# Performance work log

Hardware: AMD Instinct MI355X
Metric: run time of the kernel (lower is better)

The kernel has to match this reference:

```python
import jax, jax.numpy as jnp
import numpy as np

H = 256       # hiddenDim
E = 300       # embDim
VOCAB = 50000
S = 1024      # number of sentences in document
L = 64        # words per sentence (chain-tree depth)
TOPIC = 100
TARGET = 5


def setup_inputs() -> dict:
    key = jax.random.key(0)
    ks = jax.random.split(key, 21)
    f32 = jnp.float32
    return {
        'sentenceInIndex': jax.random.randint(ks[0], (S, L), 0, VOCAB),
        'depTypes': jax.random.randint(ks[1], (S, L - 1), 0, 9),
        'D_T_distr': jax.random.uniform(ks[2], (TOPIC,), dtype=f32),
        'h0': jax.random.normal(ks[3], (H,), dtype=f32),
        'idx2vec': jax.random.normal(ks[4], (VOCAB, E), dtype=f32) * 0.1,
        'q': jax.random.normal(ks[5], (10, H), dtype=f32) * 0.1,
        'W': jax.random.normal(ks[6], (3 * H, E), dtype=f32) * 0.05,
        'U': jax.random.normal(ks[7], (3 * H, H), dtype=f32) * 0.05,
        'D': jax.random.normal(ks[8], (3 * H, H), dtype=f32) * 0.05,
        'b': jax.random.normal(ks[9], (3 * H,), dtype=f32) * 0.05,
        'gru_wih': jax.random.normal(ks[10], (3 * H, H), dtype=f32) * 0.05,
        'gru_whh': jax.random.normal(ks[11], (3 * H, H), dtype=f32) * 0.05,
        'gru_bih': jax.random.normal(ks[12], (3 * H,), dtype=f32) * 0.05,
        'gru_bhh': jax.random.normal(ks[13], (3 * H,), dtype=f32) * 0.05,
        'gate_W': jax.random.normal(ks[14], (2 * H, H), dtype=f32) * 0.05,
        'gate_U': jax.random.normal(ks[15], (2 * H, H), dtype=f32) * 0.05,
        'gate_b': jax.random.normal(ks[16], (2 * H,), dtype=f32) * 0.05,
        'mlp_W': jax.random.normal(ks[17], (H, TOPIC), dtype=f32) * 0.05,
        'mlp_b': jax.random.normal(ks[18], (H,), dtype=f32) * 0.05,
        'out_W': jax.random.normal(ks[19], (TARGET, H), dtype=f32) * 0.05,
        'out_b': jax.random.normal(ks[20], (TARGET,), dtype=f32) * 0.05,
    }


def reference(sentenceInIndex, depTypes, D_T_distr, h0, idx2vec, q, W, U, D, b,
              gru_wih, gru_whh, gru_bih, gru_bhh,
              gate_W, gate_U, gate_b, mlp_W, mlp_b, out_W, out_b):
    # ---- DERNN over chain-canonicalized dependency trees (vectorized over S sentences) ----
    x = idx2vec[sentenceInIndex]                        # [S, L, E] gather
    Wx = jnp.einsum('sle,ke->slk', x, W)                # [S, L, 3H]
    qe = q[depTypes]                                    # [S, L-1, H] dep-type embeddings for edges k->k+1
    Dq = jnp.einsum('slh,kh->slk', qe, D)               # [S, L-1, 3H]

    # leaf node (position L-1): q_sum = q[-1] ('leafNotion'); no child h term
    dq_leaf = D @ q[-1]                                 # [3H]
    iu_leaf = Wx[:, -1, H:] + dq_leaf[H:] + b[H:]       # [S, 2H]
    h = jnp.tanh(jax.nn.sigmoid(iu_leaf[:, :H]) * jnp.tanh(iu_leaf[:, H:]))  # [S, H]

    # internal nodes k = L-2 .. 0, single child k+1 (edge k)
    pre = Wx[:, :L - 1] + Dq + b                        # [S, L-1, 3H]
    pre_rev = jnp.swapaxes(pre[:, ::-1], 0, 1)          # [L-1, S, 3H] bottom-up order

    def tree_step(h_c, pre_k):
        tot = pre_k + h_c @ U.T                         # [S, 3H]
        f = jax.nn.sigmoid(tot[:, :H]) * h_c            # child forget gate * child h (single child => sum)
        i = jax.nn.sigmoid(tot[:, H:2 * H])
        u = jnp.tanh(tot[:, 2 * H:])
        h_n = jnp.tanh(i * u + f)
        return h_n, None

    sentenceVector, _ = jax.lax.scan(tree_step, h, pre_rev)  # [S, H] root hidden per sentence

    # ---- GRU over sentence sequence (batch 1), torch nn.GRU math ----
    def gru_step(hh, xt):
        gi = gru_wih @ xt + gru_bih                     # [3H]
        gh = gru_whh @ hh + gru_bhh
        r = jax.nn.sigmoid(gi[:H] + gh[:H])
        z = jax.nn.sigmoid(gi[H:2 * H] + gh[H:2 * H])
        n = jnp.tanh(gi[2 * H:] + r * gh[2 * H:])
        return (1.0 - z) * n + z * hh, None

    hT, _ = jax.lax.scan(gru_step, h0, sentenceVector)  # [H] final hidden state

    # ---- topic vector, GATE fusion, classifier ----
    t = jnp.tanh(mlp_W @ D_T_distr + mlp_b)             # [H]
    g = gate_W @ hT + gate_U @ t + gate_b               # [2H]
    v = jnp.tanh(jax.nn.sigmoid(g[:H]) * hT + jax.nn.sigmoid(g[H:]) * t)
    return jax.nn.softmax(out_W @ v + out_b)            # [TARGET]
```

## Files before the change

kernel.cpp:

```cpp
#include <hip/hip_runtime.h>

typedef short short8 __attribute__((ext_vector_type(8)));
typedef float f4 __attribute__((ext_vector_type(4)));
typedef int i4 __attribute__((ext_vector_type(4)));
typedef _Float16 half8 __attribute__((ext_vector_type(8)));
typedef _Float16 h2 __attribute__((ext_vector_type(2)));

#define HD 256
#define ED 300
#define EP 320
#define TH 768
#define NS 1024
#define LW 64
#define SH 4.5f

__device__ __forceinline__ unsigned short f2bf(float f) {
    unsigned int u = __float_as_uint(f);
    u = (u + 0x7FFFu + ((u >> 16) & 1u)) >> 16;
    return (unsigned short)u;
}
__device__ __forceinline__ float bf2f(unsigned short s) {
    return __uint_as_float(((unsigned int)s) << 16);
}
__device__ __forceinline__ float sigm(float x) {
    return __builtin_amdgcn_rcpf(1.f + __expf(-x));
}
__device__ __forceinline__ float tanh_(float x) {
    x = fminf(fmaxf(x, -15.f), 15.f);
    return 1.f - 2.f * __builtin_amdgcn_rcpf(1.f + __expf(2.f * x));
}
__device__ __forceinline__ unsigned int pack_h2(float a, float b) {
    h2 p; p.x = (_Float16)a; p.y = (_Float16)b;
    return __builtin_bit_cast(unsigned int, p);
}

__device__ __forceinline__ void load8bf(const unsigned short* p, float* o) {
    uint4 a = *(const uint4*)p;
    o[0] = bf2f((unsigned short)(a.x & 0xffff)); o[1] = bf2f((unsigned short)(a.x >> 16));
    o[2] = bf2f((unsigned short)(a.y & 0xffff)); o[3] = bf2f((unsigned short)(a.y >> 16));
    o[4] = bf2f((unsigned short)(a.z & 0xffff)); o[5] = bf2f((unsigned short)(a.z >> 16));
    o[6] = bf2f((unsigned short)(a.w & 0xffff)); o[7] = bf2f((unsigned short)(a.w >> 16));
}
__device__ __forceinline__ void ubf4(uint2 a, float* o) {
    o[0] = bf2f((unsigned short)(a.x & 0xffff)); o[1] = bf2f((unsigned short)(a.x >> 16));
    o[2] = bf2f((unsigned short)(a.y & 0xffff)); o[3] = bf2f((unsigned short)(a.y >> 16));
}

__global__ void k_prep(const float* __restrict__ W, const float* __restrict__ U,
                       const float* __restrict__ Wih, const float* __restrict__ Whh,
                       const float* __restrict__ q, const float* __restrict__ Dm,
                       const float* __restrict__ DT, const float* __restrict__ mlpW,
                       const float* __restrict__ mlpb,
                       const float* __restrict__ bih, const float* __restrict__ bhh,
                       unsigned short* __restrict__ Wb, _Float16* __restrict__ Uh,
                       _Float16* __restrict__ Wihh,
                       signed char* __restrict__ Wq, float* __restrict__ rowscale,
                       float* __restrict__ bias2,
                       float* __restrict__ Dq, float* __restrict__ tv) {
    __shared__ float smax[4];
    int bid = blockIdx.x, tid = threadIdx.x;
    if (bid < 768) {
        int r = bid;
        for (int j = tid; j < EP; j += 256)
            Wb[r * EP + j] = (j < ED) ? f2bf(W[r * ED + j]) : (unsigned short)0;
        float whv = Whh[r * HD + tid];
        for (int j = tid; j < HD; j += 256) {
            Uh[r * HD + j] = (_Float16)U[r * HD + j];
            Wihh[r * HD + j] = (_Float16)Wih[r * HD + j];
        }
        float v = fabsf(whv);
        for (int o = 32; o; o >>= 1) v = fmaxf(v, __shfl_xor(v, o));
        if ((tid & 63) == 0) smax[tid >> 6] = v;
        __syncthreads();
        float am = fmaxf(fmaxf(smax[0], smax[1]), fmaxf(smax[2], smax[3]));
        float inv = (am > 0.f) ? 127.f / am : 0.f;
        int qi = (int)rintf(whv * inv);
        qi = max(-127, min(127, qi));
        Wq[r * HD + tid] = (signed char)qi;
        if (tid == 0) rowscale[r] = (am / 127.f) * (SH / 127.f);
    } else if (bid < 798) {
        int idx = bid - 768;
        int d = idx / 3, part = idx - d * 3;
        int n = part * 256 + tid;
        float s = 0.f;
        for (int h = 0; h < HD; ++h) s += Dm[n * HD + h] * q[d * HD + h];
        Dq[d * TH + n] = s;
    } else {
        if (tid < HD) {
            float s = 0.f;
            for (int k = 0; k < 100; ++k) s += mlpW[tid * 100 + k] * DT[k];
            tv[tid] = tanh_(s + mlpb[tid]);
        }
        for (int r = tid; r < TH; r += 256)
            bias2[r] = bih[r] + ((r < 512) ? bhh[r] : 0.f);
    }
}

#define XP 328
__launch_bounds__(256, 2)
__global__ void k_phaseB(const int* __restrict__ sIdx, const int* __restrict__ depT,
                         const float* __restrict__ emb, const unsigned short* __restrict__ Wb,
                         const float* __restrict__ Dq, const float* __restrict__ bias,
                         unsigned short* __restrict__ pre) {
    __shared__ float dq_s[10 * 772];
    __shared__ float b_s[TH];
    __shared__ int dep_s[32];
    __shared__ int idx_s[32];
    __shared__ __align__(16) unsigned short xbf[32 * XP];
    int tid = threadIdx.x;
    int c0 = blockIdx.x * 32;
    for (int i = tid; i < 10 * 768; i += 256) {
        int d = i / 768, n = i - d * 768;
        dq_s[d * 772 + n] = Dq[i];
    }
    for (int i = tid; i < TH; i += 256) b_s[i] = bias[i];
    if (tid < 32) {
        int m = c0 + tid;
        idx_s[tid] = sIdx[m];
        int l = m & 63, s = m >> 6;
        dep_s[tid] = (l == 63) ? 9 : depT[s * 63 + l];
    }
    __syncthreads();
    for (int i = tid; i < 32 * EP; i += 256) {
        int row = i / EP, col = i - row * EP;
        unsigned short v = 0;
        if (col < ED) v = f2bf(emb[(long)idx_s[row] * ED + col]);
        xbf[row * XP + col] = v;
    }
    __syncthreads();

    int lane = tid & 63;
    int w = tid >> 6;
    int quad = lane >> 4, l16 = lane & 15;

    f4 acc[2][12];
#pragma unroll
    for (int cs = 0; cs < 2; ++cs)
#pragma unroll
        for (int ms = 0; ms < 12; ++ms) acc[cs][ms] = (f4){0.f, 0.f, 0.f, 0.f};

    const unsigned short* wbase = Wb + (w * 192 + l16) * EP;

#pragma unroll
    for (int kt = 0; kt < 10; ++kt) {
        int k0 = kt * 32 + quad * 8;
        short8 bf0 = *(const short8*)&xbf[l16 * XP + k0];
        short8 bf1 = *(const short8*)&xbf[(16 + l16) * XP + k0];
#pragma unroll
        for (int ms = 0; ms < 12; ++ms) {
            short8 af = *(const short8*)(wbase + ms * 16 * EP + k0);
            acc[0][ms] = __builtin_amdgcn_mfma_f32_16x16x32_bf16(af, bf0, acc[0][ms], 0, 0, 0);
            acc[1][ms] = __builtin_amdgcn_mfma_f32_16x16x32_bf16(af, bf1, acc[1][ms], 0, 0, 0);
        }
    }

#pragma unroll
    for (int cs = 0; cs < 2; ++cs) {
        int xr = c0 + cs * 16 + l16;
        int dep = dep_s[cs * 16 + l16];
        unsigned short* prow = pre + (long)xr * TH;
#pragma unroll
        for (int ms = 0; ms < 12; ++ms) {
            int ncol = w * 192 + ms * 16 + quad * 4;
            f4 dq4 = *(const f4*)&dq_s[dep * 772 + ncol];
            f4 b4 = *(const f4*)&b_s[ncol];
            unsigned int lo = (unsigned int)f2bf(acc[cs][ms][0] + dq4[0] + b4[0]) |
                              ((unsigned int)f2bf(acc[cs][ms][1] + dq4[1] + b4[1]) << 16);
            unsigned int hi = (unsigned int)f2bf(acc[cs][ms][2] + dq4[2] + b4[2]) |
                              ((unsigned int)f2bf(acc[cs][ms][3] + dq4[3] + b4[3]) << 16);
            uint2 v; v.x = lo; v.y = hi;
            *(uint2*)(prow + ncol) = v;
        }
    }
}

__global__ void __launch_bounds__(768) k_phaseC(
                         const unsigned short* __restrict__ pre,
                         const _Float16* __restrict__ Uh,
                         const _Float16* __restrict__ Wihh,
                         const float* __restrict__ bias2,
                         float* __restrict__ gi) {
    __shared__ __align__(16) uint4 hfr[512];
    __shared__ __align__(16) float tot[16 * 772];
    int tid = threadIdx.x;
    int lane = tid & 63, w = tid >> 6, quad = lane >> 4, l16 = lane & 15;
    int s0 = blockIdx.x * 16;

    uint4 frag[32];
    {
        const _Float16* base = Uh + (w * 64 + l16) * HD;
#pragma unroll
        for (int t = 0; t < 4; ++t)
#pragma unroll
            for (int kt = 0; kt < 8; ++kt)
                frag[t * 8 + kt] = *(const uint4*)(base + t * 16 * HD + kt * 32 + quad * 8);
    }

    int us = tid >> 5;
    int jg = tid & 31;
    int j0 = jg * 8;
    int hcell = (j0 >> 5) * 64 + 16 * ((j0 >> 3) & 3) + us;
    uint4 hcp;

    if (tid < 512) {
        const unsigned short* prow = pre + ((long)(s0 + us) * LW + 63) * TH;
        float iv[8], uv[8], hcv[8];
        load8bf(prow + 256 + j0, iv);
        load8bf(prow + 512 + j0, uv);
#pragma unroll
        for (int r = 0; r < 8; ++r) hcv[r] = tanh_(sigm(iv[r]) * tanh_(uv[r]));
        hcp.x = pack_h2(hcv[0], hcv[1]); hcp.y = pack_h2(hcv[2], hcv[3]);
        hcp.z = pack_h2(hcv[4], hcv[5]); hcp.w = pack_h2(hcv[6], hcv[7]);
        hfr[hcell] = hcp;
    }
    __syncthreads();

    int mb = w * 64 + quad * 4;

    for (int step = 0; step < 63; ++step) {
        int l = 62 - step;
        uint2 praw[6];
        if (tid < 512) {
            const unsigned short* prow = pre + ((long)(s0 + us) * LW + l) * TH;
#pragma unroll
            for (int g = 0; g < 3; ++g) {
                praw[2 * g]     = *(const uint2*)(prow + g * 256 + j0);
                praw[2 * g + 1] = *(const uint2*)(prow + g * 256 + j0 + 4);
            }
        }
        f4 a0 = (f4){0,0,0,0}, a1 = (f4){0,0,0,0}, a2 = (f4){0,0,0,0}, a3 = (f4){0,0,0,0};
#pragma unroll
        for (int kt = 0; kt < 8; ++kt) {
            half8 b = __builtin_bit_cast(half8, hfr[kt * 64 + lane]);
            a0 = __builtin_amdgcn_mfma_f32_16x16x32_f16(__builtin_bit_cast(half8, frag[kt]), b, a0, 0, 0, 0);
            a1 = __builtin_amdgcn_mfma_f32_16x16x32_f16(__builtin_bit_cast(half8, frag[8 + kt]), b, a1, 0, 0, 0);
            a2 = __builtin_amdgcn_mfma_f32_16x16x32_f16(__builtin_bit_cast(half8, frag[16 + kt]), b, a2, 0, 0, 0);
            a3 = __builtin_amdgcn_mfma_f32_16x16x32_f16(__builtin_bit_cast(half8, frag[24 + kt]), b, a3, 0, 0, 0);
        }
        float* tr = tot + l16 * 772;
        *(f4*)&tr[mb] = a0;
        *(f4*)&tr[mb + 16] = a1;
        *(f4*)&tr[mb + 32] = a2;
        *(f4*)&tr[mb + 48] = a3;
        __syncthreads();
        if (tid < 512) {
            const float* ts = tot + us * 772;
            float hcv[8];
            h2 px = __builtin_bit_cast(h2, hcp.x); h2 py = __builtin_bit_cast(h2, hcp.y);
            h2 pz = __builtin_bit_cast(h2, hcp.z); h2 pw = __builtin_bit_cast(h2, hcp.w);
            hcv[0] = (float)px.x; hcv[1] = (float)px.y; hcv[2] = (float)py.x; hcv[3] = (float)py.y;
            hcv[4] = (float)pz.x; hcv[5] = (float)pz.y; hcv[6] = (float)pw.x; hcv[7] = (float)pw.y;
#pragma unroll
            for (int hf = 0; hf < 2; ++hf) {
                int jb = j0 + hf * 4;
                float pf[4], pi_[4], pu[4];
                ubf4(praw[hf], pf);
                ubf4(praw[2 + hf], pi_);
                ubf4(praw[4 + hf], pu);
                f4 tf = *(const f4*)&ts[jb];
                f4 ti = *(const f4*)&ts[256 + jb];
                f4 tu = *(const f4*)&ts[512 + jb];
#pragma unroll
                for (int r = 0; r < 4; ++r) {
                    float ff = tf[r] + pf[r];
                    float ii = ti[r] + pi_[r];
                    float uu = tu[r] + pu[r];
                    hcv[hf * 4 + r] = tanh_(sigm(ii) * tanh_(uu) + sigm(ff) * hcv[hf * 4 + r]);
                }
            }
            hcp.x = pack_h2(hcv[0], hcv[1]); hcp.y = pack_h2(hcv[2], hcv[3]);
            hcp.z = pack_h2(hcv[4], hcv[5]); hcp.w = pack_h2(hcv[6], hcv[7]);
            hfr[hcell] = hcp;
        }
        __syncthreads();
    }

    {
        const _Float16* base = Wihh + (w * 64 + l16) * HD;
#pragma unroll
        for (int t = 0; t < 4; ++t)
#pragma unroll
            for (int kt = 0; kt < 8; ++kt)
                frag[t * 8 + kt] = *(const uint4*)(base + t * 16 * HD + kt * 32 + quad * 8);
    }
    f4 a0 = (f4){0,0,0,0}, a1 = (f4){0,0,0,0}, a2 = (f4){0,0,0,0}, a3 = (f4){0,0,0,0};
#pragma unroll
    for (int kt = 0; kt < 8; ++kt) {
        half8 b = __builtin_bit_cast(half8, hfr[kt * 64 + lane]);
        a0 = __builtin_amdgcn_mfma_f32_16x16x32_f16(__builtin_bit_cast(half8, frag[kt]), b, a0, 0, 0, 0);
        a1 = __builtin_amdgcn_mfma_f32_16x16x32_f16(__builtin_bit_cast(half8, frag[8 + kt]), b, a1, 0, 0, 0);
        a2 = __builtin_amdgcn_mfma_f32_16x16x32_f16(__builtin_bit_cast(half8, frag[16 + kt]), b, a2, 0, 0, 0);
        a3 = __builtin_amdgcn_mfma_f32_16x16x32_f16(__builtin_bit_cast(half8, frag[24 + kt]), b, a3, 0, 0, 0);
    }
    float* go = gi + (long)(s0 + l16) * TH;
    f4 b0 = *(const f4*)(bias2 + mb);
    f4 b1 = *(const f4*)(bias2 + mb + 16);
    f4 b2 = *(const f4*)(bias2 + mb + 32);
    f4 b3 = *(const f4*)(bias2 + mb + 48);
    *(f4*)(go + mb) = a0 + b0;
    *(f4*)(go + mb + 16) = a1 + b1;
    *(f4*)(go + mb + 32) = a2 + b2;
    *(f4*)(go + mb + 48) = a3 + b3;
}

__global__ void __launch_bounds__(512) k_gru(
                      const signed char* __restrict__ Wq, const float* __restrict__ rowscale,
                      const float* __restrict__ bhh,
                      const float* __restrict__ gi, const float* __restrict__ h0,
                      const float* __restrict__ tv,
                      const float* __restrict__ gateW, const float* __restrict__ gateU,
                      const float* __restrict__ gateb,
                      const float* __restrict__ outW, const float* __restrict__ outb,
                      float* __restrict__ out) {
    __shared__ __align__(16) signed char qbuf[2][HD];
    __shared__ float hts[HD];
    __shared__ float sgs[512];
    __shared__ float vvs[HD];
    __shared__ float lg[8];

    int tid = threadIdx.x;
    int lane = tid & 63, w = tid >> 6, quad = lane >> 4, l16 = lane & 15;

    i4 far_[2][4], faz[2][4], fan[2][4];
#pragma unroll
    for (int c = 0; c < 2; ++c) {
        const signed char* qr_ = Wq + (long)(w * 32 + c * 16 + l16) * HD;
        const signed char* qz_ = Wq + (long)(256 + w * 32 + c * 16 + l16) * HD;
        const signed char* qn_ = Wq + (long)(512 + w * 32 + c * 16 + l16) * HD;
#pragma unroll
        for (int kc = 0; kc < 4; ++kc) {
            far_[c][kc] = *(const i4*)(qr_ + kc * 64 + quad * 16);
            faz[c][kc] = *(const i4*)(qz_ + kc * 64 + quad * 16);
            fan[c][kc] = *(const i4*)(qn_ + kc * 64 + quad * 16);
        }
    }

    int sc = (l16 >> 2) & 1;
    int sr = l16 & 3;
    int j = w * 32 + sc * 16 + quad * 4 + sr;
    bool b2 = (sr & 2) != 0, b1 = (sr & 1) != 0, bc = (sc != 0);
    bool owner = (l16 < 8);

    float rs_r = rowscale[j];
    float rs_z = rowscale[256 + j];
    float rs_n = rowscale[512 + j];
    float bn_l = bhh[512 + j];

    float hv = h0[j];
    if (owner) {
        float hc = fminf(fmaxf(hv, -SH), SH);
        qbuf[0][j] = (signed char)(int)rintf(hc * (127.f / SH));
    }
    __syncthreads();

    const float* gbase = gi + j;
    for (int t = 0; t < NS; ++t) {
        int p = t & 1;
        const float* g = gbase + (long)t * TH;
        float gr_l = g[0], gz_l = g[256], gn_l = g[512];

        i4 qr[2], qz[2], qn[2];
#pragma unroll
        for (int c = 0; c < 2; ++c) { qr[c] = (i4){0,0,0,0}; qz[c] = (i4){0,0,0,0}; qn[c] = (i4){0,0,0,0}; }
#pragma unroll
        for (int kc = 0; kc < 4; ++kc) {
            i4 b = *(const i4*)&qbuf[p][kc * 64 + quad * 16];
            qr[0] = __builtin_amdgcn_mfma_i32_16x16x64_i8(far_[0][kc], b, qr[0], 0, 0, 0);
            qr[1] = __builtin_amdgcn_mfma_i32_16x16x64_i8(far_[1][kc], b, qr[1], 0, 0, 0);
            qz[0] = __builtin_amdgcn_mfma_i32_16x16x64_i8(faz[0][kc], b, qz[0], 0, 0, 0);
            qz[1] = __builtin_amdgcn_mfma_i32_16x16x64_i8(faz[1][kc], b, qz[1], 0, 0, 0);
            qn[0] = __builtin_amdgcn_mfma_i32_16x16x64_i8(fan[0][kc], b, qn[0], 0, 0, 0);
            qn[1] = __builtin_amdgcn_mfma_i32_16x16x64_i8(fan[1][kc], b, qn[1], 0, 0, 0);
        }
        int ra0 = bc ? qr[1][0] : qr[0][0], ra1 = bc ? qr[1][1] : qr[0][1];
        int ra2 = bc ? qr[1][2] : qr[0][2], ra3 = bc ? qr[1][3] : qr[0][3];
        int rt0 = b2 ? ra2 : ra0, rt1 = b2 ? ra3 : ra1;
        int qrv = b1 ? rt1 : rt0;
        int za0 = bc ? qz[1][0] : qz[0][0], za1 = bc ? qz[1][1] : qz[0][1];
        int za2 = bc ? qz[1][2] : qz[0][2], za3 = bc ? qz[1][3] : qz[0][3];
        int zt0 = b2 ? za2 : za0, zt1 = b2 ? za3 : za1;
        int qzv = b1 ? zt1 : zt0;
        int na0 = bc ? qn[1][0] : qn[0][0], na1 = bc ? qn[1][1] : qn[0][1];
        int na2 = bc ? qn[1][2] : qn[0][2], na3 = bc ? qn[1][3] : qn[0][3];
        int nt0 = b2 ? na2 : na0, nt1 = b2 ? na3 : na1;
        int qnv = b1 ? nt1 : nt0;
        float rv = sigm(gr_l + (float)qrv * rs_r);
        float zv = sigm(gz_l + (float)qzv * rs_z);
        float nv = tanh_(gn_l + rv * ((float)qnv * rs_n + bn_l));
        hv = (1.f - zv) * nv + zv * hv;
        if (owner) {
            float hc = fminf(fmaxf(hv, -SH), SH);
            qbuf[p ^ 1][j] = (signed char)(int)rintf(hc * (127.f / SH));
        }
        __syncthreads();
    }

    if (owner) hts[j] = hv;
    __syncthreads();
    {
        float s = gateb[tid];
        for (int k = 0; k < HD; ++k)
            s += gateW[tid * HD + k] * hts[k] + gateU[tid * HD + k] * tv[k];
        sgs[tid] = sigm(s);
    }
    __syncthreads();
    if (tid < HD) vvs[tid] = tanh_(sgs[tid] * hts[tid] + sgs[256 + tid] * tv[tid]);
    __syncthreads();
    if (tid < 5) {
        float s = outb[tid];
        for (int k = 0; k < HD; ++k) s += outW[tid * HD + k] * vvs[k];
        lg[tid] = s;
    }
    __syncthreads();
    if (tid == 0) {
        float m = lg[0];
        for (int i = 1; i < 5; ++i) m = fmaxf(m, lg[i]);
        float e[5], sum = 0.f;
        for (int i = 0; i < 5; ++i) { e[i] = __expf(lg[i] - m); sum += e[i]; }
        for (int i = 0; i < 5; ++i) out[i] = e[i] / sum;
    }
}

extern "C" void kernel_launch(void* const* d_in, const int* in_sizes, int n_in,
                              void* d_out, int out_size, void* d_ws, size_t ws_size,
                              hipStream_t stream) {
    (void)in_sizes; (void)n_in; (void)out_size; (void)ws_size;
    const int* sIdx = (const int*)d_in[0];
    const int* depT = (const int*)d_in[1];
    const float* DT = (const float*)d_in[2];
    const float* h0 = (const float*)d_in[3];
    const float* emb = (const float*)d_in[4];
    const float* q = (const float*)d_in[5];
    const float* W = (const float*)d_in[6];
    const float* U = (const float*)d_in[7];
    const float* Dm = (const float*)d_in[8];
    const float* b = (const float*)d_in[9];
    const float* Wih = (const float*)d_in[10];
    const float* Whh = (const float*)d_in[11];
    const float* bih = (const float*)d_in[12];
    const float* bhh = (const float*)d_in[13];
    const float* gateW = (const float*)d_in[14];
    const float* gateU = (const float*)d_in[15];
    const float* gateb = (const float*)d_in[16];
    const float* mlpW = (const float*)d_in[17];
    const float* mlpb = (const float*)d_in[18];
    const float* outW = (const float*)d_in[19];
    const float* outb = (const float*)d_in[20];

    char* ws = (char*)d_ws;
    unsigned short* Wb = (unsigned short*)ws;   ws += 768 * 320 * 2;
    _Float16* Uh = (_Float16*)ws;               ws += 768 * 256 * 2;
    _Float16* Wihh = (_Float16*)ws;             ws += 768 * 256 * 2;
    signed char* Wq = (signed char*)ws;         ws += 768 * 256;
    float* rowscale = (float*)ws;               ws += 768 * 4;
    float* bias2 = (float*)ws;                  ws += 768 * 4;
    float* Dq = (float*)ws;                     ws += 10 * 768 * 4;
    float* tv = (float*)ws;                     ws += 1024;
    ws = (char*)d_ws + ((((size_t)(ws - (char*)d_ws)) + 4095) & ~(size_t)4095);
    unsigned short* pre = (unsigned short*)ws;  ws += (size_t)65536 * 768 * 2;
    float* gi = (float*)ws;                     ws += (size_t)1024 * 768 * 4;

    k_prep<<<dim3(799), dim3(256), 0, stream>>>(W, U, Wih, Whh, q, Dm, DT, mlpW, mlpb,
                                                bih, bhh,
                                                Wb, Uh, Wihh, Wq, rowscale, bias2, Dq, tv);
    k_phaseB<<<dim3(2048), dim3(256), 0, stream>>>(sIdx, depT, emb, Wb, Dq, b, pre);
    k_phaseC<<<dim3(64), dim3(768), 0, stream>>>(pre, Uh, Wihh, bias2, gi);
    k_gru<<<dim3(1), dim3(512), 0, stream>>>(Wq, rowscale, bhh, gi, h0, tv,
                                             gateW, gateU, gateb, outW, outb, (float*)d_out);
}
```

Baseline: 1.311 ms.

## Replace MFMA int8 GRU recurrence with per-row sdot4 dot products across 768 threads

```diff
diff --git a/kernel.cpp b/kernel.cpp
--- a/kernel.cpp
+++ b/kernel.cpp
@@ -44,6 +44,19 @@
 __device__ __forceinline__ void ubf4(uint2 a, float* o) {
     o[0] = bf2f((unsigned short)(a.x & 0xffff)); o[1] = bf2f((unsigned short)(a.x >> 16));
     o[2] = bf2f((unsigned short)(a.y & 0xffff)); o[3] = bf2f((unsigned short)(a.y >> 16));
+}
+
+__device__ __forceinline__ int dot4(int a, int b, int c) {
+#if __has_builtin(__builtin_amdgcn_sdot4)
+    return __builtin_amdgcn_sdot4(a, b, c, false);
+#else
+    int s = c;
+    s += (int)(signed char)(a & 0xff)        * (int)(signed char)(b & 0xff);
+    s += (int)(signed char)((a >> 8) & 0xff) * (int)(signed char)((b >> 8) & 0xff);
+    s += (int)(signed char)((a >> 16) & 0xff)* (int)(signed char)((b >> 16) & 0xff);
+    s += (int)(signed char)((a >> 24) & 0xff)* (int)(signed char)((b >> 24) & 0xff);
+    return s;
+#endif
 }
 
 __global__ void k_prep(const float* __restrict__ W, const float* __restrict__ U,
@@ -303,7 +316,7 @@
     *(f4*)(go + mb + 48) = a3 + b3;
 }
 
-__global__ void __launch_bounds__(512) k_gru(
+__global__ void __launch_bounds__(768) k_gru(
                       const signed char* __restrict__ Wq, const float* __restrict__ rowscale,
                       const float* __restrict__ bhh,
                       const float* __restrict__ gi, const float* __restrict__ h0,
@@ -312,92 +325,66 @@
                       const float* __restrict__ gateb,
                       const float* __restrict__ outW, const float* __restrict__ outb,
                       float* __restrict__ out) {
-    __shared__ __align__(16) signed char qbuf[2][HD];
+    __shared__ __align__(16) int qd[2][64];
+    __shared__ float sums[TH];
+    __shared__ float gns[HD];
     __shared__ float hts[HD];
     __shared__ float sgs[512];
     __shared__ float vvs[HD];
     __shared__ float lg[8];
 
     int tid = threadIdx.x;
-    int lane = tid & 63, w = tid >> 6, quad = lane >> 4, l16 = lane & 15;
-
-    i4 far_[2][4], faz[2][4], fan[2][4];
-#pragma unroll
-    for (int c = 0; c < 2; ++c) {
-        const signed char* qr_ = Wq + (long)(w * 32 + c * 16 + l16) * HD;
-        const signed char* qz_ = Wq + (long)(256 + w * 32 + c * 16 + l16) * HD;
-        const signed char* qn_ = Wq + (long)(512 + w * 32 + c * 16 + l16) * HD;
-#pragma unroll
-        for (int kc = 0; kc < 4; ++kc) {
-            far_[c][kc] = *(const i4*)(qr_ + kc * 64 + quad * 16);
-            faz[c][kc] = *(const i4*)(qz_ + kc * 64 + quad * 16);
-            fan[c][kc] = *(const i4*)(qn_ + kc * 64 + quad * 16);
-        }
-    }
-
-    int sc = (l16 >> 2) & 1;
-    int sr = l16 & 3;
-    int j = w * 32 + sc * 16 + quad * 4 + sr;
-    bool b2 = (sr & 2) != 0, b1 = (sr & 1) != 0, bc = (sc != 0);
-    bool owner = (l16 < 8);
-
-    float rs_r = rowscale[j];
-    float rs_z = rowscale[256 + j];
-    float rs_n = rowscale[512 + j];
-    float bn_l = bhh[512 + j];
-
-    float hv = h0[j];
+    int row = tid;
+    bool isn = (row >= 512);
+    bool owner = (row < HD);
+
+    i4 wv[16];
+    {
+        const signed char* wr = Wq + (long)row * HD;
+#pragma unroll
+        for (int c = 0; c < 16; ++c) wv[c] = *(const i4*)(wr + c * 16);
+    }
+    float rs = rowscale[row];
+    float bn = isn ? bhh[row] : 0.f;
+
+    float hv = owner ? h0[row] : 0.f;
     if (owner) {
         float hc = fminf(fmaxf(hv, -SH), SH);
-        qbuf[0][j] = (signed char)(int)rintf(hc * (127.f / SH));
-    }
-    __syncthreads();
-
-    const float* gbase = gi + j;
+        ((signed char*)qd[0])[row] = (signed char)(int)rintf(hc * (127.f / SH));
+    }
+    __syncthreads();
+
+    const float* gbase = gi + row;
     for (int t = 0; t < NS; ++t) {
         int p = t & 1;
-        const float* g = gbase + (long)t * TH;
-        float gr_l = g[0], gz_l = g[256], gn_l = g[512];
-
-        i4 qr[2], qz[2], qn[2];
-#pragma unroll
-        for (int c = 0; c < 2; ++c) { qr[c] = (i4){0,0,0,0}; qz[c] = (i4){0,0,0,0}; qn[c] = (i4){0,0,0,0}; }
-#pragma unroll
-        for (int kc = 0; kc < 4; ++kc) {
-            i4 b = *(const i4*)&qbuf[p][kc * 64 + quad * 16];
-            qr[0] = __builtin_amdgcn_mfma_i32_16x16x64_i8(far_[0][kc], b, qr[0], 0, 0, 0);
-            qr[1] = __builtin_amdgcn_mfma_i32_16x16x64_i8(far_[1][kc], b, qr[1], 0, 0, 0);
-            qz[0] = __builtin_amdgcn_mfma_i32_16x16x64_i8(faz[0][kc], b, qz[0], 0, 0, 0);
-            qz[1] = __builtin_amdgcn_mfma_i32_16x16x64_i8(faz[1][kc], b, qz[1], 0, 0, 0);
-            qn[0] = __builtin_amdgcn_mfma_i32_16x16x64_i8(fan[0][kc], b, qn[0], 0, 0, 0);
-            qn[1] = __builtin_amdgcn_mfma_i32_16x16x64_i8(fan[1][kc], b, qn[1], 0, 0, 0);
-        }
-        int ra0 = bc ? qr[1][0] : qr[0][0], ra1 = bc ? qr[1][1] : qr[0][1];
-        int ra2 = bc ? qr[1][2] : qr[0][2], ra3 = bc ? qr[1][3] : qr[0][3];
-        int rt0 = b2 ? ra2 : ra0, rt1 = b2 ? ra3 : ra1;
-        int qrv = b1 ? rt1 : rt0;
-        int za0 = bc ? qz[1][0] : qz[0][0], za1 = bc ? qz[1][1] : qz[0][1];
-        int za2 = bc ? qz[1][2] : qz[0][2], za3 = bc ? qz[1][3] : qz[0][3];
-        int zt0 = b2 ? za2 : za0, zt1 = b2 ? za3 : za1;
-        int qzv = b1 ? zt1 : zt0;
-        int na0 = bc ? qn[1][0] : qn[0][0], na1 = bc ? qn[1][1] : qn[0][1];
-        int na2 = bc ? qn[1][2] : qn[0][2], na3 = bc ? qn[1][3] : qn[0][3];
-        int nt0 = b2 ? na2 : na0, nt1 = b2 ? na3 : na1;
-        int qnv = b1 ? nt1 : nt0;
-        float rv = sigm(gr_l + (float)qrv * rs_r);
-        float zv = sigm(gz_l + (float)qzv * rs_z);
-        float nv = tanh_(gn_l + rv * ((float)qnv * rs_n + bn_l));
-        hv = (1.f - zv) * nv + zv * hv;
+        float gv = gbase[(long)t * TH];
+        int acc = 0;
+#pragma unroll
+        for (int c = 0; c < 16; ++c) {
+            i4 hb = *(const i4*)&qd[p][c * 4];
+            acc = dot4(hb[0], wv[c][0], acc);
+            acc = dot4(hb[1], wv[c][1], acc);
+            acc = dot4(hb[2], wv[c][2], acc);
+            acc = dot4(hb[3], wv[c][3], acc);
+        }
+        float fv = (float)acc * rs;
+        sums[row] = isn ? (fv + bn) : (fv + gv);
+        if (isn) gns[row - 512] = gv;
+        __syncthreads();
         if (owner) {
+            float rv = sigm(sums[row]);
+            float zv = sigm(sums[HD + row]);
+            float nv = tanh_(gns[row] + rv * sums[512 + row]);
+            hv = (1.f - zv) * nv + zv * hv;
             float hc = fminf(fmaxf(hv, -SH), SH);
-            qbuf[p ^ 1][j] = (signed char)(int)rintf(hc * (127.f / SH));
+            ((signed char*)qd[p ^ 1])[row] = (signed char)(int)rintf(hc * (127.f / SH));
         }
         __syncthreads();
     }
 
-    if (owner) hts[j] = hv;
-    __syncthreads();
-    {
+    if (owner) hts[row] = hv;
+    __syncthreads();
+    if (tid < 512) {
         float s = gateb[tid];
         for (int k = 0; k < HD; ++k)
             s += gateW[tid * HD + k] * hts[k] + gateU[tid * HD + k] * tv[k];
@@ -465,6 +452,6 @@
                                                 Wb, Uh, Wihh, Wq, rowscale, bias2, Dq, tv);
     k_phaseB<<<dim3(2048), dim3(256), 0, stream>>>(sIdx, depT, emb, Wb, Dq, b, pre);
     k_phaseC<<<dim3(64), dim3(768), 0, stream>>>(pre, Uh, Wihh, bias2, gi);
-    k_gru<<<dim3(1), dim3(512), 0, stream>>>(Wq, rowscale, bhh, gi, h0, tv,
+    k_gru<<<dim3(1), dim3(768), 0, stream>>>(Wq, rowscale, bhh, gi, h0, tv,
                                              gateW, gateU, gateb, outW, outb, (float*)d_out);
 }
```

Result: slower. 1.689 ms (+28.9%).

## Prefetch GRU input gates in double-buffered LDS blocks; coalesce phaseB stores via LDS

Applied to the files above, without the earlier changes.

```diff
diff --git a/kernel.cpp b/kernel.cpp
--- a/kernel.cpp
+++ b/kernel.cpp
@@ -107,6 +107,7 @@
     __shared__ int dep_s[32];
     __shared__ int idx_s[32];
     __shared__ __align__(16) unsigned short xbf[32 * XP];
+    __shared__ __align__(16) unsigned short tbuf[16 * 776];
     int tid = threadIdx.x;
     int c0 = blockIdx.x * 32;
     for (int i = tid; i < 10 * 768; i += 256) {
@@ -156,9 +157,7 @@
 
 #pragma unroll
     for (int cs = 0; cs < 2; ++cs) {
-        int xr = c0 + cs * 16 + l16;
         int dep = dep_s[cs * 16 + l16];
-        unsigned short* prow = pre + (long)xr * TH;
 #pragma unroll
         for (int ms = 0; ms < 12; ++ms) {
             int ncol = w * 192 + ms * 16 + quad * 4;
@@ -169,8 +168,17 @@
             unsigned int hi = (unsigned int)f2bf(acc[cs][ms][2] + dq4[2] + b4[2]) |
                               ((unsigned int)f2bf(acc[cs][ms][3] + dq4[3] + b4[3]) << 16);
             uint2 v; v.x = lo; v.y = hi;
-            *(uint2*)(prow + ncol) = v;
-        }
+            *(uint2*)&tbuf[l16 * 776 + ncol] = v;
+        }
+        __syncthreads();
+        for (int it = 0; it < 6; ++it) {
+            int flat = it * 256 + tid;
+            int row = flat / 96;
+            int ch = flat - row * 96;
+            uint4 v = *(const uint4*)&tbuf[row * 776 + ch * 8];
+            *(uint4*)(pre + (long)(c0 + cs * 16 + row) * TH + ch * 8) = v;
+        }
+        __syncthreads();
     }
 }
 
@@ -303,6 +311,7 @@
     *(f4*)(go + mb + 48) = a3 + b3;
 }
 
+#define GB 8
 __global__ void __launch_bounds__(512) k_gru(
                       const signed char* __restrict__ Wq, const float* __restrict__ rowscale,
                       const float* __restrict__ bhh,
@@ -313,6 +322,7 @@
                       const float* __restrict__ outW, const float* __restrict__ outb,
                       float* __restrict__ out) {
     __shared__ __align__(16) signed char qbuf[2][HD];
+    __shared__ __align__(16) float gbuf[2][GB * TH];
     __shared__ float hts[HD];
     __shared__ float sgs[512];
     __shared__ float vvs[HD];
@@ -351,48 +361,65 @@
         float hc = fminf(fmaxf(hv, -SH), SH);
         qbuf[0][j] = (signed char)(int)rintf(hc * (127.f / SH));
     }
-    __syncthreads();
-
-    const float* gbase = gi + j;
-    for (int t = 0; t < NS; ++t) {
-        int p = t & 1;
-        const float* g = gbase + (long)t * TH;
-        float gr_l = g[0], gz_l = g[256], gn_l = g[512];
-
-        i4 qr[2], qz[2], qn[2];
-#pragma unroll
-        for (int c = 0; c < 2; ++c) { qr[c] = (i4){0,0,0,0}; qz[c] = (i4){0,0,0,0}; qn[c] = (i4){0,0,0,0}; }
-#pragma unroll
-        for (int kc = 0; kc < 4; ++kc) {
-            i4 b = *(const i4*)&qbuf[p][kc * 64 + quad * 16];
-            qr[0] = __builtin_amdgcn_mfma_i32_16x16x64_i8(far_[0][kc], b, qr[0], 0, 0, 0);
-            qr[1] = __builtin_amdgcn_mfma_i32_16x16x64_i8(far_[1][kc], b, qr[1], 0, 0, 0);
-            qz[0] = __builtin_amdgcn_mfma_i32_16x16x64_i8(faz[0][kc], b, qz[0], 0, 0, 0);
-            qz[1] = __builtin_amdgcn_mfma_i32_16x16x64_i8(faz[1][kc], b, qz[1], 0, 0, 0);
-            qn[0] = __builtin_amdgcn_mfma_i32_16x16x64_i8(fan[0][kc], b, qn[0], 0, 0, 0);
-            qn[1] = __builtin_amdgcn_mfma_i32_16x16x64_i8(fan[1][kc], b, qn[1], 0, 0, 0);
-        }
-        int ra0 = bc ? qr[1][0] : qr[0][0], ra1 = bc ? qr[1][1] : qr[0][1];
-        int ra2 = bc ? qr[1][2] : qr[0][2], ra3 = bc ? qr[1][3] : qr[0][3];
-        int rt0 = b2 ? ra2 : ra0, rt1 = b2 ? ra3 : ra1;
-        int qrv = b1 ? rt1 : rt0;
-        int za0 = bc ? qz[1][0] : qz[0][0], za1 = bc ? qz[1][1] : qz[0][1];
-        int za2 = bc ? qz[1][2] : qz[0][2], za3 = bc ? qz[1][3] : qz[0][3];
-        int zt0 = b2 ? za2 : za0, zt1 = b2 ? za3 : za1;
-        int qzv = b1 ? zt1 : zt0;
-        int na0 = bc ? qn[1][0] : qn[0][0], na1 = bc ? qn[1][1] : qn[0][1];
-        int na2 = bc ? qn[1][2] : qn[0][2], na3 = bc ? qn[1][3] : qn[0][3];
-        int nt0 = b2 ? na2 : na0, nt1 = b2 ? na3 : na1;
-        int qnv = b1 ? nt1 : nt0;
-        float rv = sigm(gr_l + (float)qrv * rs_r);
-        float zv = sigm(gz_l + (float)qzv * rs_z);
-        float nv = tanh_(gn_l + rv * ((float)qnv * rs_n + bn_l));
-        hv = (1.f - zv) * nv + zv * hv;
-        if (owner) {
-            float hc = fminf(fmaxf(hv, -SH), SH);
-            qbuf[p ^ 1][j] = (signed char)(int)rintf(hc * (127.f / SH));
-        }
-        __syncthreads();
+    float rg[12];
+#pragma unroll
+    for (int i = 0; i < 12; ++i) gbuf[0][i * 512 + tid] = gi[i * 512 + tid];
+#pragma unroll
+    for (int i = 0; i < 12; ++i) rg[i] = gi[GB * TH + i * 512 + tid];
+    __syncthreads();
+
+    for (int nb = 0; nb < NS / GB; ++nb) {
+        int buf = nb & 1;
+#pragma unroll
+        for (int u = 0; u < GB; ++u) {
+            if (u == 0) {
+#pragma unroll
+                for (int i = 0; i < 12; ++i) gbuf[buf ^ 1][i * 512 + tid] = rg[i];
+                if (nb + 2 < NS / GB) {
+                    const float* gsrc = gi + (long)(nb + 2) * GB * TH;
+#pragma unroll
+                    for (int i = 0; i < 12; ++i) rg[i] = gsrc[i * 512 + tid];
+                }
+            }
+            const int p = u & 1;
+            const float* gl = &gbuf[buf][u * TH];
+            float gr_l = gl[j], gz_l = gl[256 + j], gn_l = gl[512 + j];
+
+            i4 qr[2], qz[2], qn[2];
+#pragma unroll
+            for (int c = 0; c < 2; ++c) { qr[c] = (i4){0,0,0,0}; qz[c] = (i4){0,0,0,0}; qn[c] = (i4){0,0,0,0}; }
+#pragma unroll
+            for (int kc = 0; kc < 4; ++kc) {
+                i4 b = *(const i4*)&qbuf[p][kc * 64 + quad * 16];
+                qr[0] = __builtin_amdgcn_mfma_i32_16x16x64_i8(far_[0][kc], b, qr[0], 0, 0, 0);
+                qr[1] = __builtin_amdgcn_mfma_i32_16x16x64_i8(far_[1][kc], b, qr[1], 0, 0, 0);
+                qz[0] = __builtin_amdgcn_mfma_i32_16x16x64_i8(faz[0][kc], b, qz[0], 0, 0, 0);
+                qz[1] = __builtin_amdgcn_mfma_i32_16x16x64_i8(faz[1][kc], b, qz[1], 0, 0, 0);
+                qn[0] = __builtin_amdgcn_mfma_i32_16x16x64_i8(fan[0][kc], b, qn[0], 0, 0, 0);
+                qn[1] = __builtin_amdgcn_mfma_i32_16x16x64_i8(fan[1][kc], b, qn[1], 0, 0, 0);
+            }
+            int ra0 = bc ? qr[1][0] : qr[0][0], ra1 = bc ? qr[1][1] : qr[0][1];
+            int ra2 = bc ? qr[1][2] : qr[0][2], ra3 = bc ? qr[1][3] : qr[0][3];
+            int rt0 = b2 ? ra2 : ra0, rt1 = b2 ? ra3 : ra1;
+            int qrv = b1 ? rt1 : rt0;
+            int za0 = bc ? qz[1][0] : qz[0][0], za1 = bc ? qz[1][1] : qz[0][1];
+            int za2 = bc ? qz[1][2] : qz[0][2], za3 = bc ? qz[1][3] : qz[0][3];
+            int zt0 = b2 ? za2 : za0, zt1 = b2 ? za3 : za1;
+            int qzv = b1 ? zt1 : zt0;
+            int na0 = bc ? qn[1][0] : qn[0][0], na1 = bc ? qn[1][1] : qn[0][1];
+            int na2 = bc ? qn[1][2] : qn[0][2], na3 = bc ? qn[1][3] : qn[0][3];
+            int nt0 = b2 ? na2 : na0, nt1 = b2 ? na3 : na1;
+            int qnv = b1 ? nt1 : nt0;
+            float rv = sigm(gr_l + (float)qrv * rs_r);
+            float zv = sigm(gz_l + (float)qzv * rs_z);
+            float nv = tanh_(gn_l + rv * ((float)qnv * rs_n + bn_l));
+            hv = (1.f - zv) * nv + zv * hv;
+            if (owner) {
+                float hc = fminf(fmaxf(hv, -SH), SH);
+                qbuf[p ^ 1][j] = (signed char)(int)rintf(hc * (127.f / SH));
+            }
+            __syncthreads();
+        }
     }
 
     if (owner) hts[j] = hv;
```

Result: faster. 1.207 ms (-7.9%).
